# Kernel optimization log

Measured on AMD Instinct MI355X. Metric: run time of the kernel, lower is better.

The kernel has to match this reference:

```python
import jax, jax.numpy as jnp
import numpy as np
from jax import lax

SAMPLES = 1024  # matches init kwarg samples=1024


def setup_inputs() -> dict:
    key = jax.random.key(0)
    inputs = jax.random.normal(key, (4, 8192, 3), dtype=jnp.float32)  # B,N,3 point cloud
    return {"inputs": inputs}


def _dist_to(points, sel):
    # points: (B,N,3), sel: (B,3) -> (B,N) euclidean distance (same math as tf.norm on t1-t2)
    return jnp.linalg.norm(points - sel[:, None, :], axis=-1)


def reference(inputs):
    # Faithful FPS: original forms full BxNxN dist matrix; the math only ever
    # uses one row per iteration, so we compute rows on the fly (identical values).
    points = inputs  # (B,N,3)

    # ds initialized to distances from point 0 (row 0 of the dist matrix)
    ds = _dist_to(points, points[:, 0, :])  # (B,N)

    # first sample: argmax of ds, then min-update
    idx0 = jnp.argmax(ds, axis=-1)  # (B,)
    sel0 = jnp.take_along_axis(points, idx0[:, None, None], axis=1)[:, 0, :]  # (B,3)
    ds = jnp.minimum(ds, _dist_to(points, sel0))

    def step(ds, _):
        idx = jnp.argmax(ds, axis=-1)  # (B,)
        sel = jnp.take_along_axis(points, idx[:, None, None], axis=1)[:, 0, :]  # (B,3)
        ds = jnp.minimum(ds, _dist_to(points, sel))
        return ds, sel

    _, sels = lax.scan(step, ds, None, length=SAMPLES - 1)  # sels: (S-1,B,3)
    sampled = jnp.concatenate([sel0[:, None, :], jnp.transpose(sels, (1, 0, 2))], axis=1)
    return sampled  # (B,SAMPLES,3)
```

## Files before the change

### kernel.cpp

```cpp
#include <hip/hip_runtime.h>
#include <cfloat>
#include <cmath>


#define NPTS 8192
#define NSAMP 1024
#define TPB 512
#define PPT (NPTS / TPB)
#define NW (TPB / 64)

#define KEY_MERGE(CTRL)                                                               \
    do {                                                                              \
        const unsigned th = (unsigned)__builtin_amdgcn_update_dpp(0, (int)kh, (CTRL), 0xF, 0xF, true); \
        const unsigned tl = (unsigned)__builtin_amdgcn_update_dpp(0, (int)kl, (CTRL), 0xF, 0xF, true); \
        const unsigned long long tk = ((unsigned long long)th << 32) | tl;            \
        const unsigned long long pk = ((unsigned long long)kh << 32) | kl;            \
        const bool take = tk > pk;                                                    \
        kh = take ? th : kh;                                                          \
        kl = take ? tl : kl;                                                          \
    } while (0)

__global__ __launch_bounds__(TPB) void fps_kernel(const float* __restrict__ pts,
                                                  float* __restrict__ out) {
#pragma clang fp contract(off)
    const int b = blockIdx.x;
    const int tid = threadIdx.x;
    const float* __restrict__ P = pts + (size_t)b * NPTS * 3;
    float* __restrict__ O = out + (size_t)b * NSAMP * 3;

    __shared__ float4 sp4[NPTS];
    __shared__ uint2  sSlot[2][NW];

    float px[PPT], py[PPT], pz[PPT], dsq[PPT];

    const float p0x = P[0], p0y = P[1], p0z = P[2];

    float mval = -FLT_MAX, m2 = -FLT_MAX;
    int mj = 0;
#pragma unroll
    for (int j = 0; j < PPT; ++j) {
        const int i = j * TPB + tid;
        const float x = P[i * 3 + 0];
        const float y = P[i * 3 + 1];
        const float z = P[i * 3 + 2];
        px[j] = x; py[j] = y; pz[j] = z;
        sp4[i] = make_float4(x, y, z, 0.0f);
        const float dx = x - p0x, dy = y - p0y, dz = z - p0z;
        const float d = (dx * dx + dy * dy) + dz * dz;
        dsq[j] = d;
        const float t = fminf(d, mval);
        m2 = fmaxf(m2, t);
        if (d > mval) { mval = d; mj = j; }
    }
    __syncthreads();

    const int lane = tid & 63;
    const int wid  = tid >> 6;

    for (int s = 0; s < NSAMP; ++s) {
        const int buf = s & 1;

        const float sU = sqrtf(mval);
        if (m2 >= mval * 0.999999f) {
#pragma unroll
            for (int j = PPT - 1; j >= 0; --j)
                if (sqrtf(dsq[j]) == sU) mj = j;
        }
        unsigned kh = __float_as_uint(sU);
        unsigned kl = ~(unsigned)(mj * TPB + tid);

        KEY_MERGE(0x111);
        KEY_MERGE(0x112);
        KEY_MERGE(0x114);
        KEY_MERGE(0x118);
        KEY_MERGE(0x142);
        KEY_MERGE(0x143);
        if (lane == 63) sSlot[buf][wid] = make_uint2(kl, kh);
        __syncthreads();

        const uint2 pr = sSlot[buf][lane & (NW - 1)];
        kl = pr.x; kh = pr.y;
        KEY_MERGE(0x124);
        KEY_MERGE(0x122);
        KEY_MERGE(0x121);

        const int gidx = (int)(~kl);
        const float4 c = sp4[gidx];
        const float sx = c.x, sy = c.y, sz = c.z;

        if (tid == 0) {
            O[s * 3 + 0] = sx;
            O[s * 3 + 1] = sy;
            O[s * 3 + 2] = sz;
        }

        mval = -FLT_MAX; m2 = -FLT_MAX; mj = 0;
#pragma unroll
        for (int j = 0; j < PPT; ++j) {
            const float dx = px[j] - sx;
            const float dy = py[j] - sy;
            const float dz = pz[j] - sz;
            const float nd = (dx * dx + dy * dy) + dz * dz;
            const float d  = fminf(dsq[j], nd);
            dsq[j] = d;
            const float t = fminf(d, mval);
            m2 = fmaxf(m2, t);
            if (d > mval) { mval = d; mj = j; }
        }
    }
}

extern "C" void kernel_launch(void* const* d_in, const int* in_sizes, int n_in,
                              void* d_out, int out_size, void* d_ws, size_t ws_size,
                              hipStream_t stream) {
    const float* pts = (const float*)d_in[0];
    float* out = (float*)d_out;
    const int B = in_sizes[0] / (NPTS * 3);
    fps_kernel<<<B, TPB, 0, stream>>>(pts, out);
}
```

Baseline: 1.220 ms.

## Halve block size, merge wave slots by vector LDS read, buffer output in LDS

Drops the block from 512 to 256 threads (4 waves, 32 points per thread), so the cross-wave reduction reads all four slot keys with two 128-bit LDS loads and reduces them with scalar 64-bit compares instead of three DPP merge steps. Sampled coordinates are staged in shared memory and written to global memory in one coalesced pass at the end. With only 4 batches launched, fewer threads per block means fewer active SIMDs per CU and more serial distance work per thread, traded against a cheaper barrier and reduction in each of the 1024 iterations.

```diff
diff --git a/kernel.cpp b/kernel.cpp
--- a/kernel.cpp
+++ b/kernel.cpp
@@ -5,7 +5,7 @@
 
 #define NPTS 8192
 #define NSAMP 1024
-#define TPB 512
+#define TPB 256
 #define PPT (NPTS / TPB)
 #define NW (TPB / 64)
 
@@ -29,7 +29,8 @@
     float* __restrict__ O = out + (size_t)b * NSAMP * 3;
 
     __shared__ float4 sp4[NPTS];
-    __shared__ uint2  sSlot[2][NW];
+    __shared__ float  sOut[NSAMP * 3];
+    __shared__ __align__(16) uint2 sSlot[2][NW];
 
     float px[PPT], py[PPT], pz[PPT], dsq[PPT];
 
@@ -78,20 +79,25 @@
         if (lane == 63) sSlot[buf][wid] = make_uint2(kl, kh);
         __syncthreads();
 
-        const uint2 pr = sSlot[buf][lane & (NW - 1)];
-        kl = pr.x; kh = pr.y;
-        KEY_MERGE(0x124);
-        KEY_MERGE(0x122);
-        KEY_MERGE(0x121);
+        const uint4* sl = reinterpret_cast<const uint4*>(&sSlot[buf][0]);
+        const uint4 a = sl[0];
+        const uint4 c4 = sl[1];
+        const unsigned long long K0 = ((unsigned long long)a.y  << 32) | a.x;
+        const unsigned long long K1 = ((unsigned long long)a.w  << 32) | a.z;
+        const unsigned long long K2 = ((unsigned long long)c4.y << 32) | c4.x;
+        const unsigned long long K3 = ((unsigned long long)c4.w << 32) | c4.z;
+        const unsigned long long m01 = K0 > K1 ? K0 : K1;
+        const unsigned long long m23 = K2 > K3 ? K2 : K3;
+        const unsigned long long K   = m01 > m23 ? m01 : m23;
 
-        const int gidx = (int)(~kl);
+        const int gidx = (int)(~(unsigned)K);
         const float4 c = sp4[gidx];
         const float sx = c.x, sy = c.y, sz = c.z;
 
         if (tid == 0) {
-            O[s * 3 + 0] = sx;
-            O[s * 3 + 1] = sy;
-            O[s * 3 + 2] = sz;
+            sOut[s * 3 + 0] = sx;
+            sOut[s * 3 + 1] = sy;
+            sOut[s * 3 + 2] = sz;
         }
 
         mval = -FLT_MAX; m2 = -FLT_MAX; mj = 0;
@@ -108,6 +114,11 @@
             if (d > mval) { mval = d; mj = j; }
         }
     }
+
+    __syncthreads();
+#pragma unroll
+    for (int k = tid; k < NSAMP * 3; k += TPB)
+        O[k] = sOut[k];
 }
 
 extern "C" void kernel_launch(void* const* d_in, const int* in_sizes, int n_in,
```

New measurement: 1.147 ms. 6.0% less time.
